# Performance work log

Hardware: AMD Instinct MI355X
Metric: run time of the kernel (lower is better)

Reference implementation:

```python
import jax, jax.numpy as jnp
import numpy as np

N_HEADS = 16


def setup_inputs() -> dict:
    key = jax.random.key(0)
    ks = jax.random.split(key, 5)
    B, S, D = 2, 2048, 1024
    scale = 1.0 / np.sqrt(D)
    return {
        "x": jax.random.normal(ks[0], (B, S, D), dtype=jnp.float32),
        "w_in": jax.random.normal(ks[1], (3 * D, D), dtype=jnp.float32) * scale,
        "b_in": jax.random.normal(ks[2], (3 * D,), dtype=jnp.float32) * 0.01,
        "w_out": jax.random.normal(ks[3], (D, D), dtype=jnp.float32) * scale,
        "b_out": jax.random.normal(ks[4], (D,), dtype=jnp.float32) * 0.01,
        "mask": 1,
    }


def reference(x, w_in, b_in, w_out, b_out, mask):
    b, s, d = x.shape
    h = N_HEADS
    dh = d // h
    # fused QKV projection (torch Linear: x @ W^T + b)
    qkv = jnp.einsum("bsd,ed->bse", x, w_in) + b_in  # [b, s, 3d]
    q, k, v = jnp.split(qkv, 3, axis=-1)
    # [b, s, d] -> [b, h, s, dh]
    q = q.reshape(b, s, h, dh).transpose(0, 2, 1, 3)
    k = k.reshape(b, s, h, dh).transpose(0, 2, 1, 3)
    v = v.reshape(b, s, h, dh).transpose(0, 2, 1, 3)
    att = jnp.einsum("bhqd,bhkd->bhqk", q, k)
    if mask:
        causal = jnp.triu(jnp.ones((s, s), dtype=bool), k=1)
        att = jnp.where(causal, -jnp.inf, att)
    att = att / jnp.sqrt(jnp.asarray(dh, att.dtype))
    att = jax.nn.softmax(att, axis=-1)
    out = jnp.einsum("bhqk,bhkd->bhqd", att, v)  # [b, h, s, dh]
    out = out.transpose(0, 2, 1, 3).reshape(b, s, d)
    return jnp.einsum("bsd,ed->bse", out, w_out) + b_out
```

## Files before the change

kernel.cpp:

```cpp
#include <hip/hip_runtime.h>
#include <hip/hip_bf16.h>
#include <cmath>

typedef __hip_bfloat16 bf16;
typedef short v8s __attribute__((ext_vector_type(8)));
typedef short v4s __attribute__((ext_vector_type(4)));
typedef float v4f __attribute__((ext_vector_type(4)));

#define AS1(p) ((__attribute__((address_space(1))) void*)(p))
#define AS3(p) ((__attribute__((address_space(3))) void*)(p))

__device__ __forceinline__ v4f mfma_bf16(v8s a, v8s b, v4f c) {
    return __builtin_amdgcn_mfma_f32_16x16x32_bf16(a, b, c, 0, 0, 0);
}

__device__ __forceinline__ short bf16_bits(float f) {
    return __builtin_bit_cast(short, __float2bfloat16(f));
}

__global__ __launch_bounds__(256)
void cvt_all(const float* __restrict__ x, const float* __restrict__ w_in,
             const float* __restrict__ w_out, bf16* __restrict__ xb,
             bf16* __restrict__ wib, bf16* __restrict__ wob)
{
    const int i = blockIdx.x * 256 + threadIdx.x;
    const float* src; bf16* dst; int j;
    if (i < 1048576)      { src = x;     dst = xb;  j = i; }
    else if (i < 1835008) { src = w_in;  dst = wib; j = i - 1048576; }
    else                  { src = w_out; dst = wob; j = i - 1835008; }
    const float4 v = ((const float4*)src)[j];
    v4s p;
    p.x = bf16_bits(v.x); p.y = bf16_bits(v.y);
    p.z = bf16_bits(v.z); p.w = bf16_bits(v.w);
    ((v4s*)dst)[j] = p;
}

template<int NF>
__global__ __launch_bounds__(256)
void gemm_bt(const bf16* __restrict__ A, const bf16* __restrict__ Bt,
             const float* __restrict__ bias, bf16* __restrict__ C,
             float* __restrict__ Cf, int N, int K, int lda)
{
    constexpr int BN = NF * 32;
    __shared__ __align__(16) bf16 As[2][128 * 32];
    __shared__ __align__(16) bf16 Bs[2][BN * 32];

    const int t    = threadIdx.x;
    const int lane = t & 63;
    const int wave = t >> 6;
    const int l16  = lane & 15;
    const int quad = lane >> 4;
    const int m0   = blockIdx.y * 128;
    const int n0   = blockIdx.x * BN;
    const int wm   = (wave >> 1) * 64;
    const int wn   = (wave & 1) * (NF * 16);

    const v4f zf = {0.f, 0.f, 0.f, 0.f};
    v4f acc[4][NF];
#pragma unroll
    for (int i = 0; i < 4; ++i)
#pragma unroll
        for (int j = 0; j < NF; ++j) acc[i][j] = zf;

    const int sr = t >> 2;
    const int g  = ((t & 3) ^ ((sr >> 1) & 3)) * 8;
    const bf16* gA = A  + (size_t)(m0 + sr) * lda + g;
    const bf16* gB = Bt + (size_t)(n0 + sr) * K + g;

    auto stage = [&](int kt, int buf) {
        const int k0 = kt * 32;
        char* lA = (char*)&As[buf][0] + t * 16;
        char* lB = (char*)&Bs[buf][0] + t * 16;
        __builtin_amdgcn_global_load_lds(AS1(gA + k0),                    AS3(lA),        16, 0, 0);
        __builtin_amdgcn_global_load_lds(AS1(gA + (size_t)64 * lda + k0), AS3(lA + 4096), 16, 0, 0);
        __builtin_amdgcn_global_load_lds(AS1(gB + k0),                    AS3(lB),        16, 0, 0);
        if (NF == 4)
            __builtin_amdgcn_global_load_lds(AS1(gB + (size_t)64 * K + k0), AS3(lB + 4096), 16, 0, 0);
    };

    stage(0, 0);
    const int KT = K >> 5;
    const int xs = ((l16 >> 1) & 3) * 8;
    for (int kt = 0; kt < KT; ++kt) {
        const int buf = kt & 1;
        __syncthreads();
        if (kt + 1 < KT) stage(kt + 1, buf ^ 1);

        v8s af[4], bfr[NF];
#pragma unroll
        for (int mi = 0; mi < 4; ++mi)
            af[mi] = *(const v8s*)(&As[buf][0] + (wm + mi * 16 + l16) * 32
                                   + ((quad * 8) ^ xs));
#pragma unroll
        for (int ni = 0; ni < NF; ++ni)
            bfr[ni] = *(const v8s*)(&Bs[buf][0] + (wn + ni * 16 + l16) * 32
                                    + ((quad * 8) ^ xs));
#pragma unroll
        for (int mi = 0; mi < 4; ++mi)
#pragma unroll
            for (int ni = 0; ni < NF; ++ni)
                acc[mi][ni] = mfma_bf16(af[mi], bfr[ni], acc[mi][ni]);
    }

#pragma unroll
    for (int ni = 0; ni < NF; ++ni) {
        const int col = n0 + wn + ni * 16 + l16;
        const float bv = bias[col];
#pragma unroll
        for (int mi = 0; mi < 4; ++mi) {
#pragma unroll
            for (int r = 0; r < 4; ++r) {
                const int row = m0 + wm + mi * 16 + quad * 4 + r;
                const float fv = acc[mi][ni][r] + bv;
                if (Cf) Cf[(size_t)row * N + col] = fv;
                else    C [(size_t)row * N + col] = __float2bfloat16(fv);
            }
        }
    }
}

__global__ __launch_bounds__(256)
void vtrans(const bf16* __restrict__ qkv, bf16* __restrict__ Vt)
{
    __shared__ short Ts[64][72];
    const int t  = threadIdx.x;
    const int st = blockIdx.x;
    const int bh = blockIdx.y;
    const int b = bh >> 4, h = bh & 15;
    const int s0 = st * 64;
    {
        const int i = t >> 2, j0 = (t & 3) * 16;
        const bf16* src = qkv + (size_t)(b * 2048 + s0 + i) * 3072 + 2048 + h * 64 + j0;
        const v8s a0 = *(const v8s*)(src);
        const v8s a1 = *(const v8s*)(src + 8);
        *(v8s*)&Ts[i][j0]     = a0;
        *(v8s*)&Ts[i][j0 + 8] = a1;
    }
    __syncthreads();
    {
        const int d = t >> 2, seg = (t & 3) * 16;
        v8s o0, o1;
#pragma unroll
        for (int m = 0; m < 8; ++m) { o0[m] = Ts[seg + m][d]; o1[m] = Ts[seg + 8 + m][d]; }
        bf16* dst = Vt + (size_t)(bh * 64 + d) * 2048 + s0 + seg;
        *(v8s*)dst       = o0;
        *(v8s*)(dst + 8) = o1;
    }
}

#define M_STATIC 14.0f
__global__ __launch_bounds__(256)
void attn(bf16* __restrict__ qkv, const bf16* __restrict__ Vt)
{
    __shared__ __align__(16) bf16 Ks[2][64 * 64];
    __shared__ __align__(16) bf16 Vs[2][64 * 64];
    __shared__ __align__(16) short Ps[4][16 * 72];

    const int t    = threadIdx.x;
    const int lane = t & 63;
    const int w    = t >> 6;
    const int l16  = lane & 15;
    const int quad = lane >> 4;
    const int id   = blockIdx.x;
    const int bh   = id & 31;
    const int qb   = 31 - (id >> 5);
    const int b = bh >> 4, h = bh & 15;
    const int T = qb + 1;
    const int rowq = qb * 64 + w * 16;

    v8s qf[2];
    {
        const bf16* Qb = qkv + (size_t)(b * 2048 + rowq + l16) * 3072 + h * 64 + quad * 8;
        qf[0] = *(const v8s*)(Qb);
        qf[1] = *(const v8s*)(Qb + 32);
    }

    const int sr  = t >> 3;
    const int swz = ((t & 7) ^ (sr & 7)) * 8;
    const bf16* kbase = qkv + (size_t)(b * 2048 + sr) * 3072 + 1024 + h * 64 + swz;
    const bf16* vbase = Vt + (size_t)(bh * 64 + sr) * 2048 + swz;
    char* kd = (char*)&Ks[0][0] + t * 16;
    char* vd = (char*)&Vs[0][0] + t * 16;

    __builtin_amdgcn_global_load_lds(AS1(kbase),                     AS3(kd),        16, 0, 0);
    __builtin_amdgcn_global_load_lds(AS1(kbase + (size_t)32 * 3072), AS3(kd + 4096), 16, 0, 0);
    __builtin_amdgcn_global_load_lds(AS1(vbase),                     AS3(vd),        16, 0, 0);
    __builtin_amdgcn_global_load_lds(AS1(vbase + (size_t)32 * 2048), AS3(vd + 4096), 16, 0, 0);

    const v4f zf = {0.f, 0.f, 0.f, 0.f};
    v4f o[4] = {zf, zf, zf, zf};
    float lsum[4] = {0.f, 0.f, 0.f, 0.f};
    short* Pw = &Ps[w][0];
    const int xsw = (l16 & 7) * 8;

    for (int tile = 0; tile < T; ++tile) {
        const int buf = tile & 1;
        __syncthreads();
        if (tile + 1 < T) {
            const int nb = buf ^ 1;
            const bf16* ksrc = kbase + (size_t)((tile + 1) * 64) * 3072;
            const bf16* vsrc = vbase + (tile + 1) * 64;
            char* kdn = (char*)&Ks[nb][0] + t * 16;
            char* vdn = (char*)&Vs[nb][0] + t * 16;
            __builtin_amdgcn_global_load_lds(AS1(ksrc),                     AS3(kdn),        16, 0, 0);
            __builtin_amdgcn_global_load_lds(AS1(ksrc + (size_t)32 * 3072), AS3(kdn + 4096), 16, 0, 0);
            __builtin_amdgcn_global_load_lds(AS1(vsrc),                     AS3(vdn),        16, 0, 0);
            __builtin_amdgcn_global_load_lds(AS1(vsrc + (size_t)32 * 2048), AS3(vdn + 4096), 16, 0, 0);
        }

        v4f s[4] = {zf, zf, zf, zf};
#pragma unroll
        for (int ks = 0; ks < 2; ++ks)
#pragma unroll
            for (int ct = 0; ct < 4; ++ct) {
                const v8s kf = *(const v8s*)(&Ks[buf][0] + (ct * 16 + l16) * 64
                                             + (((ks * 4 + quad) * 8) ^ xsw));
                s[ct] = mfma_bf16(qf[ks], kf, s[ct]);
            }

        if (tile == T - 1) {
            const int colb = tile * 64;
            const int rowb = rowq + quad * 4;
#pragma unroll
            for (int ct = 0; ct < 4; ++ct) {
                const int col = colb + ct * 16 + l16;
#pragma unroll
                for (int r = 0; r < 4; ++r) {
                    const float p = (col > rowb + r)
                        ? 0.f : __expf(fmaf(s[ct][r], 0.125f, -M_STATIC));
                    lsum[r] += p;
                    Pw[(quad * 4 + r) * 72 + ct * 16 + l16] = bf16_bits(p);
                }
            }
        } else {
#pragma unroll
            for (int ct = 0; ct < 4; ++ct)
#pragma unroll
                for (int r = 0; r < 4; ++r) {
                    const float p = __expf(fmaf(s[ct][r], 0.125f, -M_STATIC));
                    lsum[r] += p;
                    Pw[(quad * 4 + r) * 72 + ct * 16 + l16] = bf16_bits(p);
                }
        }
        asm volatile("s_waitcnt lgkmcnt(0)" ::: "memory");

#pragma unroll
        for (int ks = 0; ks < 2; ++ks) {
            const v8s pf = *(const v8s*)(Pw + l16 * 72 + ks * 32 + quad * 8);
#pragma unroll
            for (int nt = 0; nt < 4; ++nt) {
                const v8s vf = *(const v8s*)(&Vs[buf][0] + (nt * 16 + l16) * 64
                                             + (((ks * 4 + quad) * 8) ^ xsw));
                o[nt] = mfma_bf16(pf, vf, o[nt]);
            }
        }
    }

#pragma unroll
    for (int r = 0; r < 4; ++r) {
        float l = lsum[r];
        l += __shfl_xor(l, 1); l += __shfl_xor(l, 2);
        l += __shfl_xor(l, 4); l += __shfl_xor(l, 8);
        lsum[r] = fmaxf(l, 1e-30f);
    }

#pragma unroll
    for (int nt = 0; nt < 4; ++nt)
#pragma unroll
        for (int r = 0; r < 4; ++r) {
            const int row = rowq + quad * 4 + r;
            qkv[(size_t)(b * 2048 + row) * 3072 + 2048 + h * 64 + nt * 16 + l16] =
                __float2bfloat16(o[nt][r] / lsum[r]);
        }
}

extern "C" void kernel_launch(void* const* d_in, const int* in_sizes, int n_in,
                              void* d_out, int out_size, void* d_ws, size_t ws_size,
                              hipStream_t stream)
{
    (void)in_sizes; (void)n_in; (void)out_size; (void)ws_size;
    const float* x     = (const float*)d_in[0];
    const float* w_in  = (const float*)d_in[1];
    const float* b_in  = (const float*)d_in[2];
    const float* w_out = (const float*)d_in[3];
    const float* b_out = (const float*)d_in[4];
    float* out = (float*)d_out;

    bf16* ws     = (bf16*)d_ws;
    bf16* xb     = ws;
    bf16* w_inb  = xb     + (size_t)4096 * 1024;
    bf16* w_outb = w_inb  + (size_t)3072 * 1024;
    bf16* qkv    = w_outb + (size_t)1024 * 1024;
    bf16* vt     = (bf16*)d_out;

    cvt_all<<<8192, 256, 0, stream>>>(x, w_in, w_out, xb, w_inb, w_outb);

    gemm_bt<4><<<dim3(24, 32), dim3(256), 0, stream>>>(xb, w_inb, b_in, qkv, nullptr,
                                                       3072, 1024, 1024);
    vtrans<<<dim3(32, 32), dim3(256), 0, stream>>>(qkv, vt);
    attn<<<1024, 256, 0, stream>>>(qkv, vt);
    gemm_bt<2><<<dim3(16, 32), dim3(256), 0, stream>>>(qkv + 2048, w_outb, b_out, nullptr,
                                                       out, 1024, 1024, 3072);
}
```

Baseline: 192.0 us.

## Rewrite attention with 32x32 MFMA, register-resident P, and two-wave blocks

The attention kernel moves from 16x16x32 to 32x32x16 bf16 MFMA, with each of two waves handling 32 query rows. It computes S transposed (K as the A operand) so the softmax probabilities can be packed into the PV operand in registers via cvt_pk_bf16 and permlane32_swap, which removes the LDS round trip for P. On the diagonal tile it also skips the fully masked upper 32-key half for wave 0. The cost is halving threads per block, so each block loads the K/V tiles with fewer threads, plus more register pressure from the 16-wide accumulators.

After: 197.8 us. +3.0%, slower.

```diff
diff --git a/kernel.cpp b/kernel.cpp
--- a/kernel.cpp
+++ b/kernel.cpp
@@ -6,6 +6,8 @@
 typedef short v8s __attribute__((ext_vector_type(8)));
 typedef short v4s __attribute__((ext_vector_type(4)));
 typedef float v4f __attribute__((ext_vector_type(4)));
+typedef float v16f __attribute__((ext_vector_type(16)));
+typedef unsigned v4u __attribute__((ext_vector_type(4)));
 
 #define AS1(p) ((__attribute__((address_space(1))) void*)(p))
 #define AS3(p) ((__attribute__((address_space(3))) void*)(p))
@@ -13,9 +15,17 @@
 __device__ __forceinline__ v4f mfma_bf16(v8s a, v8s b, v4f c) {
     return __builtin_amdgcn_mfma_f32_16x16x32_bf16(a, b, c, 0, 0, 0);
 }
+__device__ __forceinline__ v16f mfma32(v8s a, v8s b, v16f c) {
+    return __builtin_amdgcn_mfma_f32_32x32x16_bf16(a, b, c, 0, 0, 0);
+}
 
 __device__ __forceinline__ short bf16_bits(float f) {
     return __builtin_bit_cast(short, __float2bfloat16(f));
+}
+
+__device__ __forceinline__ v8s pack4(unsigned a, unsigned b, unsigned c, unsigned d) {
+    v4u u = {a, b, c, d};
+    return __builtin_bit_cast(v8s, u);
 }
 
 __global__ __launch_bounds__(256)
@@ -149,129 +159,136 @@
 }
 
 #define M_STATIC 14.0f
-__global__ __launch_bounds__(256)
+
+__device__ __forceinline__ void softpack(v16f s, int kg0, int qg, bool mask, int hi,
+                                         float& lsum, v8s& paE, v8s& paO)
+{
+    float p[16];
+#pragma unroll
+    for (int r = 0; r < 16; ++r) {
+        float pv = __expf(fmaf(s[r], 0.125f, -M_STATIC));
+        if (mask) {
+            const int kg = kg0 + (r & 3) + 8 * (r >> 2) + 4 * hi;
+            if (kg > qg) pv = 0.f;
+        }
+        lsum += pv;
+        p[r] = pv;
+    }
+    unsigned P0[4], P1[4];
+#pragma unroll
+    for (int m = 0; m < 4; ++m) {
+        asm("v_cvt_pk_bf16_f32 %0, %1, %2" : "=v"(P0[m]) : "v"(p[4 * m]),     "v"(p[4 * m + 1]));
+        asm("v_cvt_pk_bf16_f32 %0, %1, %2" : "=v"(P1[m]) : "v"(p[4 * m + 2]), "v"(p[4 * m + 3]));
+    }
+    auto sA = __builtin_amdgcn_permlane32_swap(P0[0], P0[1], false, false);
+    auto sB = __builtin_amdgcn_permlane32_swap(P1[0], P1[1], false, false);
+    auto sC = __builtin_amdgcn_permlane32_swap(P0[2], P0[3], false, false);
+    auto sD = __builtin_amdgcn_permlane32_swap(P1[2], P1[3], false, false);
+    paE = pack4(sA[0], sB[0], sA[1], sB[1]);
+    paO = pack4(sC[0], sD[0], sC[1], sD[1]);
+}
+
+__global__ __launch_bounds__(128)
 void attn(bf16* __restrict__ qkv, const bf16* __restrict__ Vt)
 {
     __shared__ __align__(16) bf16 Ks[2][64 * 64];
     __shared__ __align__(16) bf16 Vs[2][64 * 64];
-    __shared__ __align__(16) short Ps[4][16 * 72];
 
     const int t    = threadIdx.x;
     const int lane = t & 63;
     const int w    = t >> 6;
-    const int l16  = lane & 15;
-    const int quad = lane >> 4;
+    const int l31  = lane & 31;
+    const int hi   = lane >> 5;
     const int id   = blockIdx.x;
     const int bh   = id & 31;
     const int qb   = 31 - (id >> 5);
     const int b = bh >> 4, h = bh & 15;
     const int T = qb + 1;
-    const int rowq = qb * 64 + w * 16;
-
-    v8s qf[2];
+    const int rowq = qb * 64 + w * 32;
+    const int qg   = rowq + l31;
+    const int xr   = l31 & 7;
+
+    v8s qf[4];
     {
-        const bf16* Qb = qkv + (size_t)(b * 2048 + rowq + l16) * 3072 + h * 64 + quad * 8;
-        qf[0] = *(const v8s*)(Qb);
-        qf[1] = *(const v8s*)(Qb + 32);
+        const bf16* Qb = qkv + (size_t)(b * 2048 + qg) * 3072 + h * 64 + hi * 8;
+#pragma unroll
+        for (int c = 0; c < 4; ++c) qf[c] = *(const v8s*)(Qb + c * 16);
     }
 
     const int sr  = t >> 3;
     const int swz = ((t & 7) ^ (sr & 7)) * 8;
     const bf16* kbase = qkv + (size_t)(b * 2048 + sr) * 3072 + 1024 + h * 64 + swz;
     const bf16* vbase = Vt + (size_t)(bh * 64 + sr) * 2048 + swz;
-    char* kd = (char*)&Ks[0][0] + t * 16;
-    char* vd = (char*)&Vs[0][0] + t * 16;
-
-    __builtin_amdgcn_global_load_lds(AS1(kbase),                     AS3(kd),        16, 0, 0);
-    __builtin_amdgcn_global_load_lds(AS1(kbase + (size_t)32 * 3072), AS3(kd + 4096), 16, 0, 0);
-    __builtin_amdgcn_global_load_lds(AS1(vbase),                     AS3(vd),        16, 0, 0);
-    __builtin_amdgcn_global_load_lds(AS1(vbase + (size_t)32 * 2048), AS3(vd + 4096), 16, 0, 0);
-
-    const v4f zf = {0.f, 0.f, 0.f, 0.f};
-    v4f o[4] = {zf, zf, zf, zf};
-    float lsum[4] = {0.f, 0.f, 0.f, 0.f};
-    short* Pw = &Ps[w][0];
-    const int xsw = (l16 & 7) * 8;
+
+    auto stage = [&](int tile, int buf2) {
+        char* kd = (char*)&Ks[buf2][0] + t * 16;
+        char* vd = (char*)&Vs[buf2][0] + t * 16;
+        const bf16* ks0 = kbase + (size_t)(tile * 64) * 3072;
+        const bf16* vs0 = vbase + tile * 64;
+#pragma unroll
+        for (int i = 0; i < 4; ++i) {
+            __builtin_amdgcn_global_load_lds(AS1(ks0 + (size_t)(16 * i) * 3072), AS3(kd + i * 2048), 16, 0, 0);
+            __builtin_amdgcn_global_load_lds(AS1(vs0 + (size_t)(16 * i) * 2048), AS3(vd + i * 2048), 16, 0, 0);
+        }
+    };
+
+    stage(0, 0);
+
+    v16f o0 = {}, o1 = {};
+    float lsum = 0.f;
 
     for (int tile = 0; tile < T; ++tile) {
         const int buf = tile & 1;
         __syncthreads();
-        if (tile + 1 < T) {
-            const int nb = buf ^ 1;
-            const bf16* ksrc = kbase + (size_t)((tile + 1) * 64) * 3072;
-            const bf16* vsrc = vbase + (tile + 1) * 64;
-            char* kdn = (char*)&Ks[nb][0] + t * 16;
-            char* vdn = (char*)&Vs[nb][0] + t * 16;
-            __builtin_amdgcn_global_load_lds(AS1(ksrc),                     AS3(kdn),        16, 0, 0);
-            __builtin_amdgcn_global_load_lds(AS1(ksrc + (size_t)32 * 3072), AS3(kdn + 4096), 16, 0, 0);
-            __builtin_amdgcn_global_load_lds(AS1(vsrc),                     AS3(vdn),        16, 0, 0);
-            __builtin_amdgcn_global_load_lds(AS1(vsrc + (size_t)32 * 2048), AS3(vdn + 4096), 16, 0, 0);
-        }
-
-        v4f s[4] = {zf, zf, zf, zf};
-#pragma unroll
-        for (int ks = 0; ks < 2; ++ks)
-#pragma unroll
-            for (int ct = 0; ct < 4; ++ct) {
-                const v8s kf = *(const v8s*)(&Ks[buf][0] + (ct * 16 + l16) * 64
-                                             + (((ks * 4 + quad) * 8) ^ xsw));
-                s[ct] = mfma_bf16(qf[ks], kf, s[ct]);
+        if (tile + 1 < T) stage(tile + 1, buf ^ 1);
+
+        const bf16* Kb = &Ks[buf][0];
+        const bf16* Vb = &Vs[buf][0];
+        const bool last = (tile == T - 1);
+        const bool do1  = (!last) || (w == 1);
+
+        v16f s0 = {}, s1 = {};
+#pragma unroll
+        for (int c = 0; c < 4; ++c) {
+            const v8s kf = *(const v8s*)(Kb + l31 * 64 + (((2 * c + hi) ^ xr) * 8));
+            s0 = mfma32(kf, qf[c], s0);
+        }
+        if (do1) {
+#pragma unroll
+            for (int c = 0; c < 4; ++c) {
+                const v8s kf = *(const v8s*)(Kb + (32 + l31) * 64 + (((2 * c + hi) ^ xr) * 8));
+                s1 = mfma32(kf, qf[c], s1);
             }
-
-        if (tile == T - 1) {
-            const int colb = tile * 64;
-            const int rowb = rowq + quad * 4;
-#pragma unroll
-            for (int ct = 0; ct < 4; ++ct) {
-                const int col = colb + ct * 16 + l16;
-#pragma unroll
-                for (int r = 0; r < 4; ++r) {
-                    const float p = (col > rowb + r)
-                        ? 0.f : __expf(fmaf(s[ct][r], 0.125f, -M_STATIC));
-                    lsum[r] += p;
-                    Pw[(quad * 4 + r) * 72 + ct * 16 + l16] = bf16_bits(p);
-                }
-            }
-        } else {
-#pragma unroll
-            for (int ct = 0; ct < 4; ++ct)
-#pragma unroll
-                for (int r = 0; r < 4; ++r) {
-                    const float p = __expf(fmaf(s[ct][r], 0.125f, -M_STATIC));
-                    lsum[r] += p;
-                    Pw[(quad * 4 + r) * 72 + ct * 16 + l16] = bf16_bits(p);
-                }
-        }
-        asm volatile("s_waitcnt lgkmcnt(0)" ::: "memory");
-
-#pragma unroll
-        for (int ks = 0; ks < 2; ++ks) {
-            const v8s pf = *(const v8s*)(Pw + l16 * 72 + ks * 32 + quad * 8);
-#pragma unroll
-            for (int nt = 0; nt < 4; ++nt) {
-                const v8s vf = *(const v8s*)(&Vs[buf][0] + (nt * 16 + l16) * 64
-                                             + (((ks * 4 + quad) * 8) ^ xsw));
-                o[nt] = mfma_bf16(pf, vf, o[nt]);
-            }
-        }
-    }
-
-#pragma unroll
-    for (int r = 0; r < 4; ++r) {
-        float l = lsum[r];
-        l += __shfl_xor(l, 1); l += __shfl_xor(l, 2);
-        l += __shfl_xor(l, 4); l += __shfl_xor(l, 8);
-        lsum[r] = fmaxf(l, 1e-30f);
-    }
-
-#pragma unroll
-    for (int nt = 0; nt < 4; ++nt)
-#pragma unroll
-        for (int r = 0; r < 4; ++r) {
-            const int row = rowq + quad * 4 + r;
-            qkv[(size_t)(b * 2048 + row) * 3072 + 2048 + h * 64 + nt * 16 + l16] =
-                __float2bfloat16(o[nt][r] / lsum[r]);
-        }
+        }
+
+        v8s pa0, pa1, pa2, pa3;
+        softpack(s0, tile * 64,      qg, last, hi, lsum, pa0, pa1);
+        if (do1) softpack(s1, tile * 64 + 32, qg, last, hi, lsum, pa2, pa3);
+
+        o0 = mfma32(pa0, *(const v8s*)(Vb + l31 * 64        + (((0 + hi) ^ xr) * 8)), o0);
+        o1 = mfma32(pa0, *(const v8s*)(Vb + (32 + l31) * 64 + (((0 + hi) ^ xr) * 8)), o1);
+        o0 = mfma32(pa1, *(const v8s*)(Vb + l31 * 64        + (((2 + hi) ^ xr) * 8)), o0);
+        o1 = mfma32(pa1, *(const v8s*)(Vb + (32 + l31) * 64 + (((2 + hi) ^ xr) * 8)), o1);
+        if (do1) {
+            o0 = mfma32(pa2, *(const v8s*)(Vb + l31 * 64        + (((4 + hi) ^ xr) * 8)), o0);
+            o1 = mfma32(pa2, *(const v8s*)(Vb + (32 + l31) * 64 + (((4 + hi) ^ xr) * 8)), o1);
+            o0 = mfma32(pa3, *(const v8s*)(Vb + l31 * 64        + (((6 + hi) ^ xr) * 8)), o0);
+            o1 = mfma32(pa3, *(const v8s*)(Vb + (32 + l31) * 64 + (((6 + hi) ^ xr) * 8)), o1);
+        }
+    }
+
+    const float lt = lsum + __shfl_xor(lsum, 32);
+
+    bf16* dst0 = qkv + (size_t)(b * 2048 + rowq) * 3072 + 2048 + h * 64 + l31;
+#pragma unroll
+    for (int r = 0; r < 16; ++r) {
+        const int q = (r & 3) + 8 * (r >> 2) + 4 * hi;
+        const float rs  = fmaxf(__shfl(lt, q), 1e-30f);
+        const float inv = 1.0f / rs;
+        bf16* dst = dst0 + (size_t)q * 3072;
+        dst[0]  = __float2bfloat16(o0[r] * inv);
+        dst[32] = __float2bfloat16(o1[r] * inv);
+    }
 }
 
 extern "C" void kernel_launch(void* const* d_in, const int* in_sizes, int n_in,
@@ -298,7 +315,7 @@
     gemm_bt<4><<<dim3(24, 32), dim3(256), 0, stream>>>(xb, w_inb, b_in, qkv, nullptr,
                                                        3072, 1024, 1024);
     vtrans<<<dim3(32, 32), dim3(256), 0, stream>>>(qkv, vt);
-    attn<<<1024, 256, 0, stream>>>(qkv, vt);
+    attn<<<1024, 128, 0, stream>>>(qkv, vt);
     gemm_bt<2><<<dim3(16, 32), dim3(256), 0, stream>>>(qkv + 2048, w_outb, b_out, nullptr,
                                                        out, 1024, 1024, 3072);
 }
```
